# Performance work log

Measured on AMD Instinct MI355X. Metric: run time of the kernel, lower is better.

The kernel has to match this reference:

```python
import jax, jax.numpy as jnp
import numpy as np

AGENT_RADIUS = 0.5
SAFETY_DIST = 0.1
QP_ITERS = 300


def _qp_solve(p, G, h):
    """Batched QP: min_u 0.5 u^T u + p^T u  s.t.  G u <= h  (Q = I).
    Solved in the dual by projected gradient ascent (differentiable, fixed iters).
    p: [B,2], G: [B,m,2], h: [B,m] -> u: [B,2]
    """
    GGt = jnp.einsum('bmi,bni->bmn', G, G)                 # [B,m,m]
    q = jnp.einsum('bmi,bi->bm', G, p) + h                 # [B,m]
    # Lipschitz upper bound per sample (Frobenius norm of GG^T)
    L = jnp.sqrt(jnp.sum(GGt * GGt, axis=(1, 2))) + 1e-6   # [B]
    alpha = (1.0 / L)[:, None]

    def step(lam, _):
        grad = jnp.einsum('bmn,bn->bm', GGt, lam) + q
        lam = jnp.maximum(lam - alpha * grad, 0.0)
        return lam, None

    lam0 = jnp.zeros_like(h)
    lam, _ = jax.lax.scan(step, lam0, None, length=QP_ITERS)
    u = -p - jnp.einsum('bmi,bm->bi', G, lam)
    return u


def setup_inputs() -> dict:
    key = jax.random.key(0)
    ks = jax.random.split(key, 20)
    B, F, H1, H2 = 8192, 8, 1024, 512

    def w(k, i, o):
        return (jax.random.normal(k, (i, o), jnp.float32) / np.sqrt(i)).astype(jnp.float32)

    obs_xy = jax.random.uniform(ks[17], (8, 2), jnp.float32, -10.0, 10.0)
    obs_r = jax.random.uniform(ks[18], (8, 1), jnp.float32, 0.3, 0.8)
    return {
        'x': jax.random.normal(ks[0], (B, F), jnp.float32),
        'mean': 0.1 * jax.random.normal(ks[1], (F,), jnp.float32),
        'std': jax.random.uniform(ks[2], (F,), jnp.float32, 0.5, 1.5),
        'W1': w(ks[3], F, H1), 'b1': jnp.zeros((H1,), jnp.float32),
        'W21': w(ks[4], H1, H2), 'b21': jnp.zeros((H2,), jnp.float32),
        'W22': w(ks[5], H1, H2), 'b22': jnp.zeros((H2,), jnp.float32),
        'W23': w(ks[6], H1, H2), 'b23': jnp.zeros((H2,), jnp.float32),
        'W31': w(ks[7], H2, 2), 'b31': jnp.zeros((2,), jnp.float32),
        'W32': w(ks[8], H2, 2), 'b32': jnp.zeros((2,), jnp.float32),
        'W33': w(ks[9], H2, 1), 'b33': jnp.zeros((1,), jnp.float32),
        'obstacles': jnp.concatenate([obs_xy, obs_r], axis=1),  # [8,3] (x,y,r)
        'sgn': 1,
    }


def reference(x, mean, std, W1, b1, W21, b21, W22, b22, W23, b23,
              W31, b31, W32, b32, W33, b33, obstacles, sgn):
    B = x.shape[0]
    x0 = x * std + mean                                   # un-normalized state [B,8]

    h1 = jax.nn.relu(x @ W1 + b1)
    x21 = jax.nn.relu(h1 @ W21 + b21)
    x22 = jax.nn.relu(h1 @ W22 + b22)
    x23 = jax.nn.relu(h1 @ W23 + b23)
    x31 = x21 @ W31 + b31                                 # QP linear term p [B,2]
    x32 = 4.0 * jax.nn.sigmoid(x22 @ W32 + b32)           # CBF gains p1,p2 [B,2]
    x33 = 4.0 * jax.nn.sigmoid(x23 @ W33 + b33)           # liveness gain (unused, smg off)

    px, py, theta, v = x0[:, 0], x0[:, 1], x0[:, 2], x0[:, 3]
    st, ct = jnp.sin(theta)[:, None], jnp.cos(theta)[:, None]
    vb = v[:, None]

    # static obstacles broadcast to batch + opponent as last obstacle -> [B, m]
    ox = jnp.concatenate([jnp.broadcast_to(obstacles[:, 0][None], (B, obstacles.shape[0])), x0[:, 4:5]], axis=1)
    oy = jnp.concatenate([jnp.broadcast_to(obstacles[:, 1][None], (B, obstacles.shape[0])), x0[:, 5:6]], axis=1)
    orad = jnp.concatenate([jnp.broadcast_to(obstacles[:, 2][None], (B, obstacles.shape[0])),
                            jnp.full((B, 1), AGENT_RADIUS, x0.dtype)], axis=1)

    R = AGENT_RADIUS + orad + SAFETY_DIST
    dx = px[:, None] - ox                                  # [B,m]
    dy = py[:, None] - oy

    barrier = dx * dx + dy * dy - R * R
    barrier_dot = 2.0 * dx * vb * ct + 2.0 * dy * vb * st
    Lf2b = (2.0 * v * v)[:, None]
    LgLfbu1 = -2.0 * dx * vb * st + 2.0 * dy * vb * ct
    LgLfbu2 = 2.0 * dx * ct + 2.0 * dy * st
    G = jnp.stack([-LgLfbu1, -LgLfbu2], axis=-1)           # [B,m,2]
    p1, p2 = x32[:, 0:1], x32[:, 1:2]
    h = Lf2b + (p1 + p2) * barrier_dot + p1 * p2 * barrier # [B,m]

    u = _qp_solve(x31, G, h)                               # [B,2]
    return u
```

## Files before the change

### kernel.cpp

```cpp
#include <hip/hip_runtime.h>
#include <cstdint>
#include <cstddef>

typedef unsigned short u16;
typedef u16   u16x8  __attribute__((ext_vector_type(8)));
typedef u16   u16x4  __attribute__((ext_vector_type(4)));
typedef __bf16 bf16x8 __attribute__((ext_vector_type(8)));
typedef float f32x4  __attribute__((ext_vector_type(4)));
typedef float f32x2  __attribute__((ext_vector_type(2)));

__device__ __forceinline__ float bf2f(u16 v) {
  unsigned int u = ((unsigned int)v) << 16;
  return __builtin_bit_cast(float, u);
}
__device__ __forceinline__ u16 f2bf(float f) {
  unsigned int x = __builtin_bit_cast(unsigned int, f);
  x += 0x7fffu + ((x >> 16) & 1u);
  return (u16)(x >> 16);
}

__device__ __forceinline__ void gld_lds16(const u16* g, u16* l) {
  __builtin_amdgcn_global_load_lds(
      (const __attribute__((address_space(1))) unsigned int*)g,
      (__attribute__((address_space(3))) unsigned int*)l, 16, 0, 0);
}

__global__ __launch_bounds__(256) void k_prep(const float* __restrict__ W21,
                                              const float* __restrict__ W22,
                                              u16* __restrict__ Wt,
                                              const float* __restrict__ x,
                                              const float* __restrict__ W1,
                                              const float* __restrict__ b1,
                                              u16* __restrict__ h1,
                                              float* __restrict__ head) {
  __shared__ u16 s[64][65];
  const int b = blockIdx.x;
  if (b < 256) {
    const int mat = b >> 7;
    const int tt  = b & 127;
    const int k0  = (tt >> 3) * 64;
    const int n0  = (tt & 7) * 64;
    const float* W = mat ? W22 : W21;
    const int tx = threadIdx.x & 63;
    const int ty = threadIdx.x >> 6;
#pragma unroll
    for (int i = 0; i < 16; ++i) {
      int r = i * 4 + ty;
      s[r][tx] = f2bf(W[(size_t)(k0 + r) * 512 + n0 + tx]);
    }
    __syncthreads();
    const int nbase = mat * 512 + n0;
#pragma unroll
    for (int i = 0; i < 16; ++i) {
      int r = i * 4 + ty;
      Wt[(size_t)(nbase + r) * 1024 + k0 + tx] = s[tx][r];
    }
  } else {
    const int row0 = (b - 256) * 8;
    if (threadIdx.x < 8)
      *(f32x4*)(head + 4 * (size_t)(row0 + threadIdx.x)) = f32x4{0.f, 0.f, 0.f, 0.f};
    const int c4 = threadIdx.x * 4;
    f32x4 bv = *(const f32x4*)(b1 + c4);
    f32x4 acc[8];
#pragma unroll
    for (int r = 0; r < 8; ++r) acc[r] = bv;
#pragma unroll
    for (int f = 0; f < 8; ++f) {
      f32x4 wv = *(const f32x4*)(W1 + f * 1024 + c4);
#pragma unroll
      for (int r = 0; r < 8; ++r) {
        float xv = x[(size_t)(row0 + r) * 8 + f];
#pragma unroll
        for (int e = 0; e < 4; ++e) acc[r][e] = fmaf(xv, wv[e], acc[r][e]);
      }
    }
#pragma unroll
    for (int r = 0; r < 8; ++r) {
      u16x4 o;
#pragma unroll
      for (int e = 0; e < 4; ++e) o[e] = f2bf(fmaxf(acc[r][e], 0.f));
      *(u16x4*)(h1 + (size_t)(row0 + r) * 1024 + c4) = o;
    }
  }
}

__global__ __launch_bounds__(256) void k_gemm(const u16* __restrict__ A,
                                              const u16* __restrict__ Bt,
                                              const float* __restrict__ b21,
                                              const float* __restrict__ b22,
                                              const float* __restrict__ W31,
                                              const float* __restrict__ W32,
                                              float* __restrict__ head) {
  constexpr int K  = 1024;
  constexpr int BK = 32;
  constexpr int NT = K / BK;
  __shared__ u16 As[2][128 * 32];
  __shared__ u16 Bs[2][128 * 32];

  const int t    = threadIdx.x;
  const int row0 = blockIdx.x * 128;
  const int col0 = blockIdx.y * 128;
  const int w    = t >> 6;
  const int lane = t & 63;
  const int wr   = w >> 1, wc = w & 1;
  const int lrow = lane & 15;
  const int kq   = lane >> 4;

  const int s0 = t, s1 = 256 + t;
  const int g0c = (s0 & 3) ^ ((s0 >> 3) & 3);
  const int g1c = (s1 & 3) ^ ((s1 >> 3) & 3);
  const u16* gA0 = A  + (size_t)(row0 + (s0 >> 2)) * K + g0c * 8;
  const u16* gA1 = A  + (size_t)(row0 + (s1 >> 2)) * K + g1c * 8;
  const u16* gB0 = Bt + (size_t)(col0 + (s0 >> 2)) * K + g0c * 8;
  const u16* gB1 = Bt + (size_t)(col0 + (s1 >> 2)) * K + g1c * 8;
  const int lo0 = s0 * 8, lo1 = s1 * 8;

  const int pc = kq ^ ((lrow >> 1) & 3);

  f32x4 acc[4][4];
#pragma unroll
  for (int i = 0; i < 4; ++i)
#pragma unroll
    for (int j = 0; j < 4; ++j) acc[i][j] = f32x4{0.f, 0.f, 0.f, 0.f};

  gld_lds16(gA0, As[0] + lo0);
  gld_lds16(gA1, As[0] + lo1);
  gld_lds16(gB0, Bs[0] + lo0);
  gld_lds16(gB1, Bs[0] + lo1);

  for (int kt = 0; kt < NT; ++kt) {
    const int cur = kt & 1, nxt = cur ^ 1;
    __syncthreads();

    if (kt + 1 < NT) {
      const int ko = (kt + 1) * BK;
      gld_lds16(gA0 + ko, As[nxt] + lo0);
      gld_lds16(gA1 + ko, As[nxt] + lo1);
      gld_lds16(gB0 + ko, Bs[nxt] + lo0);
      gld_lds16(gB1 + ko, Bs[nxt] + lo1);
    }

    bf16x8 af[4], bfr[4];
#pragma unroll
    for (int i = 0; i < 4; ++i)
      af[i] = __builtin_bit_cast(bf16x8,
          *(const u16x8*)(As[cur] + (wr * 64 + i * 16 + lrow) * 32 + pc * 8));
#pragma unroll
    for (int j = 0; j < 4; ++j)
      bfr[j] = __builtin_bit_cast(bf16x8,
          *(const u16x8*)(Bs[cur] + (wc * 64 + j * 16 + lrow) * 32 + pc * 8));
#pragma unroll
    for (int i = 0; i < 4; ++i)
#pragma unroll
      for (int j = 0; j < 4; ++j)
        acc[i][j] = __builtin_amdgcn_mfma_f32_16x16x32_bf16(af[i], bfr[j], acc[i][j], 0, 0, 0);
  }

  const bool isX21 = (col0 < 512);
  const float* Wh  = isX21 ? W31 : W32;
  const int   hoff = isX21 ? 0 : 2;

  float hx[16], hy[16];
#pragma unroll
  for (int n = 0; n < 16; ++n) { hx[n] = 0.f; hy[n] = 0.f; }
#pragma unroll
  for (int j = 0; j < 4; ++j) {
    int col  = col0 + wc * 64 + j * 16 + lrow;
    int wcol = col & 511;
    f32x2 wv = *(const f32x2*)(Wh + 2 * wcol);
    float bias = isX21 ? b21[col] : b22[wcol];
#pragma unroll
    for (int i = 0; i < 4; ++i)
#pragma unroll
      for (int rr = 0; rr < 4; ++rr) {
        float v = fmaxf(acc[i][j][rr] + bias, 0.f);
        hx[i * 4 + rr] = fmaf(v, wv[0], hx[i * 4 + rr]);
        hy[i * 4 + rr] = fmaf(v, wv[1], hy[i * 4 + rr]);
      }
  }
#pragma unroll
  for (int m = 1; m <= 8; m <<= 1) {
#pragma unroll
    for (int n = 0; n < 16; ++n) {
      hx[n] += __shfl_xor(hx[n], m, 64);
      hy[n] += __shfl_xor(hy[n], m, 64);
    }
  }
  if (lrow == 0) {
#pragma unroll
    for (int i = 0; i < 4; ++i)
#pragma unroll
      for (int rr = 0; rr < 4; ++rr) {
        int row = row0 + wr * 64 + i * 16 + kq * 4 + rr;
        atomicAdd(head + 4 * (size_t)row + hoff,     hx[i * 4 + rr]);
        atomicAdd(head + 4 * (size_t)row + hoff + 1, hy[i * 4 + rr]);
      }
  }
}

__global__ __launch_bounds__(256) void k_qp(const float* __restrict__ x,
                                            const float* __restrict__ mean_,
                                            const float* __restrict__ std_,
                                            const float* __restrict__ head,
                                            const float* __restrict__ b31,
                                            const float* __restrict__ b32,
                                            const float* __restrict__ obstacles,
                                            float* __restrict__ out) {
  const int r = blockIdx.x * 256 + threadIdx.x;
  f32x4 hd = *(const f32x4*)(head + 4 * (size_t)r);
  float p0  = hd[0] + b31[0];
  float p1v = hd[1] + b31[1];
  float pp1 = 4.f / (1.f + expf(-(hd[2] + b32[0])));
  float pp2 = 4.f / (1.f + expf(-(hd[3] + b32[1])));

  const f32x4* xp = (const f32x4*)(x + (size_t)r * 8);
  f32x4 xa = xp[0], xb = xp[1];
  float px = xa[0] * std_[0] + mean_[0];
  float py = xa[1] * std_[1] + mean_[1];
  float th = xa[2] * std_[2] + mean_[2];
  float v  = xa[3] * std_[3] + mean_[3];
  float ax = xb[0] * std_[4] + mean_[4];
  float ay = xb[1] * std_[5] + mean_[5];
  float st = sinf(th), ct = cosf(th);
  float Lf2b = 2.f * v * v;

  float G0[9], G1[9], q[9];
  float s00 = 0.f, s01 = 0.f, s11 = 0.f;
#pragma unroll
  for (int m = 0; m < 9; ++m) {
    float ox, oy, orad;
    if (m < 8) {
      ox = obstacles[m * 3]; oy = obstacles[m * 3 + 1]; orad = obstacles[m * 3 + 2];
    } else { ox = ax; oy = ay; orad = 0.5f; }
    float R  = 0.6f + orad;
    float dx = px - ox, dy = py - oy;
    float bar  = dx * dx + dy * dy - R * R;
    float dct  = dx * ct + dy * st;
    float bdot = 2.f * v * dct;
    float g0 = 2.f * v * (dx * st - dy * ct);
    float g1 = -2.f * dct;
    float h  = Lf2b + (pp1 + pp2) * bdot + pp1 * pp2 * bar;
    G0[m] = g0; G1[m] = g1;
    q[m] = g0 * p0 + g1 * p1v + h;
    s00 += g0 * g0; s01 += g0 * g1; s11 += g1 * g1;
  }
  float L = sqrtf(s00 * s00 + 2.f * s01 * s01 + s11 * s11) + 1e-6f;
  float alpha = 1.f / L;

  float lam[9];
#pragma unroll
  for (int m = 0; m < 9; ++m) lam[m] = 0.f;
  for (int it = 0; it < 300; ++it) {
    float pr0[9], pr1[9];
#pragma unroll
    for (int m = 0; m < 9; ++m) { pr0[m] = G0[m] * lam[m]; pr1[m] = G1[m] * lam[m]; }
    float t0 = (((pr0[0] + pr0[1]) + (pr0[2] + pr0[3])) +
                ((pr0[4] + pr0[5]) + (pr0[6] + pr0[7]))) + pr0[8];
    float t1 = (((pr1[0] + pr1[1]) + (pr1[2] + pr1[3])) +
                ((pr1[4] + pr1[5]) + (pr1[6] + pr1[7]))) + pr1[8];
#pragma unroll
    for (int m = 0; m < 9; ++m) {
      float g = fmaf(G0[m], t0, fmaf(G1[m], t1, q[m]));
      lam[m] = fmaxf(fmaf(-alpha, g, lam[m]), 0.f);
    }
  }
  float u0 = -p0, u1 = -p1v;
#pragma unroll
  for (int m = 0; m < 9; ++m) { u0 = fmaf(-G0[m], lam[m], u0); u1 = fmaf(-G1[m], lam[m], u1); }
  *(f32x2*)(out + 2 * (size_t)r) = f32x2{u0, u1};
}

extern "C" void kernel_launch(void* const* d_in, const int* in_sizes, int n_in,
                              void* d_out, int out_size, void* d_ws, size_t ws_size,
                              hipStream_t stream) {
  const float* x    = (const float*)d_in[0];
  const float* mean_= (const float*)d_in[1];
  const float* std_ = (const float*)d_in[2];
  const float* W1   = (const float*)d_in[3];
  const float* b1   = (const float*)d_in[4];
  const float* W21  = (const float*)d_in[5];
  const float* b21  = (const float*)d_in[6];
  const float* W22  = (const float*)d_in[7];
  const float* b22  = (const float*)d_in[8];
  const float* W31  = (const float*)d_in[11];
  const float* b31  = (const float*)d_in[12];
  const float* W32  = (const float*)d_in[13];
  const float* b32  = (const float*)d_in[14];
  const float* obst = (const float*)d_in[17];
  float* out = (float*)d_out;

  char* ws = (char*)d_ws;
  u16*   Wt   = (u16*)ws;
  u16*   h1   = (u16*)(ws + (size_t)(1 << 21));
  float* head = (float*)(ws + (size_t)(1 << 21) + (size_t)(1 << 24));

  k_prep<<<256 + 1024, 256, 0, stream>>>(W21, W22, Wt, x, W1, b1, h1, head);
  k_gemm<<<dim3(64, 8), 256, 0, stream>>>(h1, Wt, b21, b22, W31, W32, head);
  k_qp  <<<32, 256, 0, stream>>>(x, mean_, std_, head, b31, b32, obst, out);
}
```

Baseline: 173.7 us.

## Load GEMM operands directly from global into registers, dropping LDS staging

The bf16 GEMM no longer stages A and B tiles through double-buffered shared memory with global_load_lds and per-tile barriers. Each wave now loads its MFMA fragments straight from global memory into registers, double-buffered in registers across two k-steps. This removes the LDS traffic and __syncthreads, but the two waves that share each row or column tile now fetch it redundantly from global/L2, and the global accesses are strided by row.

New measurement: 202.4 us. +16.5%, slower.

```diff
diff --git a/kernel.cpp b/kernel.cpp
--- a/kernel.cpp
+++ b/kernel.cpp
@@ -17,12 +17,6 @@
   unsigned int x = __builtin_bit_cast(unsigned int, f);
   x += 0x7fffu + ((x >> 16) & 1u);
   return (u16)(x >> 16);
-}
-
-__device__ __forceinline__ void gld_lds16(const u16* g, u16* l) {
-  __builtin_amdgcn_global_load_lds(
-      (const __attribute__((address_space(1))) unsigned int*)g,
-      (__attribute__((address_space(3))) unsigned int*)l, 16, 0, 0);
 }
 
 __global__ __launch_bounds__(256) void k_prep(const float* __restrict__ W21,
@@ -94,8 +88,6 @@
   constexpr int K  = 1024;
   constexpr int BK = 32;
   constexpr int NT = K / BK;
-  __shared__ u16 As[2][128 * 32];
-  __shared__ u16 Bs[2][128 * 32];
 
   const int t    = threadIdx.x;
   const int row0 = blockIdx.x * 128;
@@ -106,16 +98,14 @@
   const int lrow = lane & 15;
   const int kq   = lane >> 4;
 
-  const int s0 = t, s1 = 256 + t;
-  const int g0c = (s0 & 3) ^ ((s0 >> 3) & 3);
-  const int g1c = (s1 & 3) ^ ((s1 >> 3) & 3);
-  const u16* gA0 = A  + (size_t)(row0 + (s0 >> 2)) * K + g0c * 8;
-  const u16* gA1 = A  + (size_t)(row0 + (s1 >> 2)) * K + g1c * 8;
-  const u16* gB0 = Bt + (size_t)(col0 + (s0 >> 2)) * K + g0c * 8;
-  const u16* gB1 = Bt + (size_t)(col0 + (s1 >> 2)) * K + g1c * 8;
-  const int lo0 = s0 * 8, lo1 = s1 * 8;
-
-  const int pc = kq ^ ((lrow >> 1) & 3);
+  const u16* pa[4];
+  const u16* pb[4];
+#pragma unroll
+  for (int i = 0; i < 4; ++i)
+    pa[i] = A + (size_t)(row0 + wr * 64 + i * 16 + lrow) * K + kq * 8;
+#pragma unroll
+  for (int j = 0; j < 4; ++j)
+    pb[j] = Bt + (size_t)(col0 + wc * 64 + j * 16 + lrow) * K + kq * 8;
 
   f32x4 acc[4][4];
 #pragma unroll
@@ -123,37 +113,46 @@
 #pragma unroll
     for (int j = 0; j < 4; ++j) acc[i][j] = f32x4{0.f, 0.f, 0.f, 0.f};
 
-  gld_lds16(gA0, As[0] + lo0);
-  gld_lds16(gA1, As[0] + lo1);
-  gld_lds16(gB0, Bs[0] + lo0);
-  gld_lds16(gB1, Bs[0] + lo1);
-
-  for (int kt = 0; kt < NT; ++kt) {
-    const int cur = kt & 1, nxt = cur ^ 1;
-    __syncthreads();
-
-    if (kt + 1 < NT) {
-      const int ko = (kt + 1) * BK;
-      gld_lds16(gA0 + ko, As[nxt] + lo0);
-      gld_lds16(gA1 + ko, As[nxt] + lo1);
-      gld_lds16(gB0 + ko, Bs[nxt] + lo0);
-      gld_lds16(gB1 + ko, Bs[nxt] + lo1);
-    }
-
-    bf16x8 af[4], bfr[4];
-#pragma unroll
-    for (int i = 0; i < 4; ++i)
-      af[i] = __builtin_bit_cast(bf16x8,
-          *(const u16x8*)(As[cur] + (wr * 64 + i * 16 + lrow) * 32 + pc * 8));
-#pragma unroll
-    for (int j = 0; j < 4; ++j)
-      bfr[j] = __builtin_bit_cast(bf16x8,
-          *(const u16x8*)(Bs[cur] + (wc * 64 + j * 16 + lrow) * 32 + pc * 8));
+  u16x8 a0[4], b0[4], a1[4], b1[4];
+#pragma unroll
+  for (int i = 0; i < 4; ++i) {
+    a0[i] = *(const u16x8*)(pa[i]);
+    b0[i] = *(const u16x8*)(pb[i]);
+    a1[i] = *(const u16x8*)(pa[i] + BK);
+    b1[i] = *(const u16x8*)(pb[i] + BK);
+  }
+
+  for (int kt = 0; kt < NT; kt += 2) {
 #pragma unroll
     for (int i = 0; i < 4; ++i)
 #pragma unroll
       for (int j = 0; j < 4; ++j)
-        acc[i][j] = __builtin_amdgcn_mfma_f32_16x16x32_bf16(af[i], bfr[j], acc[i][j], 0, 0, 0);
+        acc[i][j] = __builtin_amdgcn_mfma_f32_16x16x32_bf16(
+            __builtin_bit_cast(bf16x8, a0[i]),
+            __builtin_bit_cast(bf16x8, b0[j]), acc[i][j], 0, 0, 0);
+    if (kt + 2 < NT) {
+      const int ko = (kt + 2) * BK;
+#pragma unroll
+      for (int i = 0; i < 4; ++i) {
+        a0[i] = *(const u16x8*)(pa[i] + ko);
+        b0[i] = *(const u16x8*)(pb[i] + ko);
+      }
+    }
+#pragma unroll
+    for (int i = 0; i < 4; ++i)
+#pragma unroll
+      for (int j = 0; j < 4; ++j)
+        acc[i][j] = __builtin_amdgcn_mfma_f32_16x16x32_bf16(
+            __builtin_bit_cast(bf16x8, a1[i]),
+            __builtin_bit_cast(bf16x8, b1[j]), acc[i][j], 0, 0, 0);
+    if (kt + 3 < NT) {
+      const int ko = (kt + 3) * BK;
+#pragma unroll
+      for (int i = 0; i < 4; ++i) {
+        a1[i] = *(const u16x8*)(pa[i] + ko);
+        b1[i] = *(const u16x8*)(pb[i] + ko);
+      }
+    }
   }
 
   const bool isX21 = (col0 < 512);
```
